# Performance work log

Hardware: AMD Instinct MI355X
Metric: run time of the kernel (lower is better)

## Reference

```python
import jax, jax.numpy as jnp
import numpy as np

PROJ_DIM = 128
TEMP = 0.1
CLAMP_VAL = 50.0
EPS = 1e-6


def _coords(H, W):
    # [H*W, 2] grid of (x, y) coordinates, matching torch meshgrid indexing='ij'
    xs = jnp.arange(W, dtype=jnp.float32)
    ys = jnp.arange(H, dtype=jnp.float32)
    grid_y, grid_x = jnp.meshgrid(ys, xs, indexing='ij')
    return jnp.stack([grid_x.reshape(-1), grid_y.reshape(-1)], axis=-1)


def setup_inputs() -> dict:
    key = jax.random.key(0)
    k1, k2 = jax.random.split(key)
    B, C, H, W = 2, 128, 96, 96
    fL = jax.random.normal(k1, (B, C, H, W), dtype=jnp.float32)
    fR = jax.random.normal(k2, (B, C, H, W), dtype=jnp.float32)
    return {"fL": fL, "fR": fR}


def reference(fL, fR):
    B, C, H, W = fL.shape
    HW = H * W
    scale = jnp.float32(np.sqrt(PROJ_DIM))

    # L2-normalize over channel dim with epsilon clamp
    fLn = fL / jnp.maximum(jnp.linalg.norm(fL, axis=1, keepdims=True), EPS)
    fRn = fR / jnp.maximum(jnp.linalg.norm(fR, axis=1, keepdims=True), EPS)

    q = fLn.reshape(B, C, HW).transpose(0, 2, 1).astype(jnp.float32)  # [B, HW, C]
    k = fRn.reshape(B, C, HW).astype(jnp.float32)                      # [B, C, HW]

    coords = _coords(H, W)  # [HW, 2]

    # Global correlation: [B, HW, HW] (chunking in the original is math-equivalent)
    corr = jnp.einsum('bqc,bck->bqk', q, k) / scale
    corr = jnp.clip(corr / TEMP, -CLAMP_VAL, CLAMP_VAL)
    prob = jax.nn.softmax(corr, axis=-1)

    expected_pos = prob @ coords                 # [B, HW, 2]
    max_prob = jnp.max(prob, axis=-1)            # [B, HW]

    flow_abs = expected_pos.reshape(B, H, W, 2).transpose(0, 3, 1, 2)  # [B, 2, H, W]
    conf = max_prob.reshape(B, 1, H, W)

    src = coords.reshape(H, W, 2).transpose(2, 0, 1)[None]  # [1, 2, H, W]
    flow = (flow_abs - src).astype(fL.dtype)
    conf = conf.astype(fL.dtype)
    return flow, conf
```

## Files before the change

kernel.cpp:

```cpp
#include <hip/hip_runtime.h>
#include <stdint.h>

#define HW 9216
#define CDIM 128
#define WIDTH 96
#define BATCH 2
#define SPLITS 48
#define KSPLIT 192
#define NKG 6
#define QTILE 128
#define NQT (HW / QTILE)
#define NWG (NQT * SPLITS * BATCH)

#define QSCALE 0.44194173824159216f
#define MXSCALE 2.8853900817779268f

typedef _Float16 half8 __attribute__((ext_vector_type(8)));
typedef float f32x16 __attribute__((ext_vector_type(16)));
typedef float float2v __attribute__((ext_vector_type(2)));

__global__ __launch_bounds__(256) void norm_kernel(const float* __restrict__ fL,
                                                   const float* __restrict__ fR,
                                                   _Float16* __restrict__ Qh,
                                                   _Float16* __restrict__ Kh)
{
    __shared__ float ssred[4][64];
    __shared__ _Float16 ot[64 * 130];

    const float* src = (blockIdx.y == 0) ? fL : fR;
    _Float16* dst    = (blockIdx.y == 0) ? Qh : Kh;
    const float outScale = (blockIdx.y == 0) ? QSCALE : 1.0f;

    const int t = threadIdx.x;
    const int pos_l = t & 63, cg = t >> 6;
    const int pos0 = blockIdx.x * 64;
    const int b = pos0 / HW, pos_in = pos0 % HW + pos_l;

    const float* p = src + (size_t)b * CDIM * HW + pos_in;

    float v[32];
    float ss = 0.f;
    #pragma unroll
    for (int j = 0; j < 32; ++j) {
        v[j] = p[(size_t)(cg * 32 + j) * HW];
        ss += v[j] * v[j];
    }
    ssred[cg][pos_l] = ss;
    __syncthreads();
    float tot = ssred[0][pos_l] + ssred[1][pos_l] + ssred[2][pos_l] + ssred[3][pos_l];
    float scale = outScale / fmaxf(sqrtf(tot), 1e-6f);

    #pragma unroll
    for (int j = 0; j < 32; ++j)
        ot[pos_l * 130 + cg * 32 + j] = (_Float16)(v[j] * scale);
    __syncthreads();

    uint4* og = (uint4*)(dst + (size_t)(b * HW + pos0 % HW + 0) * CDIM);
    #pragma unroll
    for (int i = 0; i < 4; ++i) {
        int idx = i * 256 + t;
        int row = idx >> 4, chunk = idx & 15;
        og[idx] = *(const uint4*)&ot[row * 130 + chunk * 8];
    }
}

__global__ __launch_bounds__(256, 3) void attn_kernel(const _Float16* __restrict__ Qh,
                                                      const _Float16* __restrict__ Kh,
                                                      float4* __restrict__ part)
{
    __shared__ __align__(16) _Float16 Ks[KSPLIT * 128];

    const int wg0 = blockIdx.x;
    const int nid = (wg0 & 7) * (NWG / 8) + (wg0 >> 3);
    const int qt = nid % NQT;
    const int sb = nid / NQT;
    const int split = sb % SPLITS;
    const int b = sb / SPLITS;

    const int t = threadIdx.x;
    const int lane = t & 63, wave = t >> 6;
    const int lane31 = lane & 31, hi = lane >> 5;
    const int ln15 = lane & 15, qd = lane >> 4;

    const char* kp0 = (const char*)(Kh + (size_t)b * HW * CDIM) +
                      (size_t)(split * KSPLIT) * (CDIM * 2);

    {
        int voff4[4];
        #pragma unroll
        for (int i = 0; i < 4; ++i) {
            int r = wave * 48 + i * 4 + qd;
            voff4[i] = r * 256 + ((ln15 ^ (r & 15)) << 4) - i * 1024;
        }
        _Float16* db = &Ks[wave * (48 * 128)];
        #pragma unroll
        for (int i = 0; i < 12; ++i)
            __builtin_amdgcn_global_load_lds(
                (const __attribute__((address_space(1))) uint32_t*)(kp0 + voff4[i & 3] + i * 1024),
                (__attribute__((address_space(3))) uint32_t*)(db + i * 512),
                16, 0, 0);
    }

    half8 qf[8];
    {
        const char* qb = (const char*)(Qh +
            ((size_t)(b * HW + qt * QTILE + wave * 32 + lane31)) * CDIM);
        #pragma unroll
        for (int kc = 0; kc < 8; ++kc)
            qf[kc] = *(const half8*)(qb + kc * 32 + hi * 16);
    }

    int rdoff[8];
    #pragma unroll
    for (int kc = 0; kc < 8; ++kc)
        rdoff[kc] = (lane31 << 8) + ((((kc << 1) | hi) ^ ln15) << 4);

    const float ysp = (float)(split * 2);

    float2v E2[8];
    #pragma unroll
    for (int p = 0; p < 8; ++p) E2[p] = (float2v)0.f;
    float mxs = -1.0e30f;
    float2v axb2 = (float2v)0.f, ay2 = (float2v)0.f;

    const char* ksb = (const char*)&Ks[0];
    const float2v C4 = (float2v)(1.0f / 24.0f), C3 = (float2v)(1.0f / 6.0f),
                  C2 = (float2v)0.5f, C1 = (float2v)1.0f;

    __syncthreads();

    #define CHAIN(ACC, KG)                                                       \
        {                                                                        \
            __builtin_amdgcn_s_setprio(1);                                       \
            _Pragma("unroll")                                                    \
            for (int kc = 0; kc < 8; ++kc) {                                     \
                half8 kf = *(const half8*)(ksb + (KG) * 8192 + rdoff[kc]);       \
                ACC = __builtin_amdgcn_mfma_f32_32x32x16_f16(                    \
                    kf, qf[kc], (kc == 0) ? (f32x16)0.f : ACC, 0, 0, 0);         \
            }                                                                    \
            __builtin_amdgcn_s_setprio(0);                                       \
        }

    #define EPI(ACC, KG)                                                         \
        {                                                                        \
            const float xb = (float)(32 * ((KG) % 3));                           \
            const float yk = ysp + (float)((KG) / 3);                            \
            float2v lt2;                                                         \
            _Pragma("unroll")                                                    \
            for (int p = 0; p < 8; ++p) {                                        \
                float2v w;                                                       \
                w.x = ACC[2 * p];                                                \
                w.y = ACC[2 * p + 1];                                            \
                mxs = fmaxf(mxs, fmaxf(w.x, w.y));           \
                float2v h = w * C4 + C3;                       \
                h = h * w + C2;                                                  \
                h = h * w + C1;                                                  \
                h = h * w + C1;                                                  \
                float2v e = h * h;                                               \
                E2[p] += e;                                                      \
                lt2 = (p == 0) ? e : (lt2 + e);                                  \
            }                                                                    \
            axb2 += lt2 * (float2v)xb;                                           \
            ay2  += lt2 * (float2v)yk;                                           \
        }

    f32x16 accA, accB;
    CHAIN(accA, 0)
    CHAIN(accB, 1) __builtin_amdgcn_sched_barrier(0); EPI(accA, 0)
    CHAIN(accA, 2) __builtin_amdgcn_sched_barrier(0); EPI(accB, 1)
    CHAIN(accB, 3) __builtin_amdgcn_sched_barrier(0); EPI(accA, 2)
    CHAIN(accA, 4) __builtin_amdgcn_sched_barrier(0); EPI(accB, 3)
    CHAIN(accB, 5) __builtin_amdgcn_sched_barrier(0); EPI(accA, 4)
    EPI(accB, 5)
    #undef CHAIN
    #undef EPI

    float l = 0.f, axc = 0.f;
    #pragma unroll
    for (int p = 0; p < 8; ++p) {
        const float c0 = (float)(((2 * p) & 3) + 8 * ((2 * p) >> 2));
        l   += E2[p].x + E2[p].y;
        axc += c0 * E2[p].x + (c0 + 1.0f) * E2[p].y;
    }
    float ax = axc + (float)(4 * hi) * l + axb2.x + axb2.y;
    float ay = ay2.x + ay2.y;
    float mx = mxs;

    l  += __shfl_xor(l, 32, 64);
    ax += __shfl_xor(ax, 32, 64);
    ay += __shfl_xor(ay, 32, 64);
    mx  = fmaxf(mx, __shfl_xor(mx, 32, 64));

    if (hi == 0) {
        int row = qt * QTILE + wave * 32 + lane31;
        part[(size_t)split * (BATCH * HW) + b * HW + row] =
            make_float4(l, ax, ay, __builtin_amdgcn_exp2f(mx * MXSCALE));
    }
}

__global__ __launch_bounds__(256) void combine_kernel(const float4* __restrict__ part,
                                                      float* __restrict__ out)
{
    int tid = blockIdx.x * 256 + threadIdx.x;
    int b = tid / HW, pos = tid % HW;
    float l = 0.f, ax = 0.f, ay = 0.f, mx = 0.f;
    #pragma unroll
    for (int s = 0; s < SPLITS; ++s) {
        float4 v = part[(size_t)s * (BATCH * HW) + tid];
        l += v.x; ax += v.y; ay += v.z; mx = fmaxf(mx, v.w);
    }
    float inv = 1.0f / l;
    int x = pos % WIDTH, y = pos / WIDTH;
    out[(size_t)b * 2 * HW + pos]           = ax * inv - (float)x;
    out[(size_t)b * 2 * HW + HW + pos]      = ay * inv - (float)y;
    out[(size_t)BATCH * 2 * HW + (size_t)b * HW + pos] = mx * inv;
}

extern "C" void kernel_launch(void* const* d_in, const int* in_sizes, int n_in,
                              void* d_out, int out_size, void* d_ws, size_t ws_size,
                              hipStream_t stream)
{
    const float* fL = (const float*)d_in[0];
    const float* fR = (const float*)d_in[1];
    float* out = (float*)d_out;

    char* ws = (char*)d_ws;
    const size_t QH_BYTES = (size_t)BATCH * HW * CDIM * sizeof(_Float16);
    _Float16* Qh  = (_Float16*)ws;
    _Float16* Kh  = (_Float16*)(ws + QH_BYTES);
    float4*   part = (float4*)(ws + 2 * QH_BYTES);

    norm_kernel<<<dim3((BATCH * HW) / 64, 2), 256, 0, stream>>>(fL, fR, Qh, Kh);
    attn_kernel<<<dim3(NWG), 256, 0, stream>>>(Qh, Kh, part);
    combine_kernel<<<dim3((BATCH * HW) / 256), 256, 0, stream>>>(part, out);
}
```

Measured before the change: 138.4 us.

## Interleave paired MFMA chains in attention and split combine reduction across waves

The attention kernel now runs two independent MFMA accumulator chains side by side (four accumulators in total) and batches the softmax epilogues into pairs. This exposes more instruction-level parallelism to hide MFMA latency, at the cost of more live registers and possibly lower occupancy. The combine kernel now spreads the 48 split partials over four waves per row group and reduces them through shared memory, launching four times as many blocks so more loads are in flight.

```diff
diff --git a/kernel.cpp b/kernel.cpp
--- a/kernel.cpp
+++ b/kernel.cpp
@@ -129,14 +129,17 @@
 
     __syncthreads();
 
-    #define CHAIN(ACC, KG)                                                       \
+    #define CHAIN2(ACCX, KGX, ACCY, KGY)                                         \
         {                                                                        \
             __builtin_amdgcn_s_setprio(1);                                       \
             _Pragma("unroll")                                                    \
             for (int kc = 0; kc < 8; ++kc) {                                     \
-                half8 kf = *(const half8*)(ksb + (KG) * 8192 + rdoff[kc]);       \
-                ACC = __builtin_amdgcn_mfma_f32_32x32x16_f16(                    \
-                    kf, qf[kc], (kc == 0) ? (f32x16)0.f : ACC, 0, 0, 0);         \
+                half8 kx = *(const half8*)(ksb + (KGX) * 8192 + rdoff[kc]);      \
+                half8 ky = *(const half8*)(ksb + (KGY) * 8192 + rdoff[kc]);      \
+                ACCX = __builtin_amdgcn_mfma_f32_32x32x16_f16(                   \
+                    kx, qf[kc], (kc == 0) ? (f32x16)0.f : ACCX, 0, 0, 0);        \
+                ACCY = __builtin_amdgcn_mfma_f32_32x32x16_f16(                   \
+                    ky, qf[kc], (kc == 0) ? (f32x16)0.f : ACCY, 0, 0, 0);        \
             }                                                                    \
             __builtin_amdgcn_s_setprio(0);                                       \
         }
@@ -164,15 +167,14 @@
             ay2  += lt2 * (float2v)yk;                                           \
         }
 
-    f32x16 accA, accB;
-    CHAIN(accA, 0)
-    CHAIN(accB, 1) __builtin_amdgcn_sched_barrier(0); EPI(accA, 0)
-    CHAIN(accA, 2) __builtin_amdgcn_sched_barrier(0); EPI(accB, 1)
-    CHAIN(accB, 3) __builtin_amdgcn_sched_barrier(0); EPI(accA, 2)
-    CHAIN(accA, 4) __builtin_amdgcn_sched_barrier(0); EPI(accB, 3)
-    CHAIN(accB, 5) __builtin_amdgcn_sched_barrier(0); EPI(accA, 4)
-    EPI(accB, 5)
-    #undef CHAIN
+    f32x16 accA, accB, accC, accD;
+    CHAIN2(accA, 0, accB, 1)
+    CHAIN2(accC, 2, accD, 3)
+    __builtin_amdgcn_sched_barrier(0); EPI(accA, 0) EPI(accB, 1)
+    CHAIN2(accA, 4, accB, 5)
+    __builtin_amdgcn_sched_barrier(0); EPI(accC, 2) EPI(accD, 3)
+    EPI(accA, 4) EPI(accB, 5)
+    #undef CHAIN2
     #undef EPI
 
     float l = 0.f, axc = 0.f;
@@ -201,19 +203,32 @@
 __global__ __launch_bounds__(256) void combine_kernel(const float4* __restrict__ part,
                                                       float* __restrict__ out)
 {
-    int tid = blockIdx.x * 256 + threadIdx.x;
-    int b = tid / HW, pos = tid % HW;
+    __shared__ float4 red[3][64];
+    const int t = threadIdx.x;
+    const int r = t & 63, g = t >> 6;
+    const int tid = blockIdx.x * 64 + r;
+    const int b = tid / HW, pos = tid % HW;
+
     float l = 0.f, ax = 0.f, ay = 0.f, mx = 0.f;
     #pragma unroll
-    for (int s = 0; s < SPLITS; ++s) {
-        float4 v = part[(size_t)s * (BATCH * HW) + tid];
+    for (int s = 0; s < 12; ++s) {
+        float4 v = part[(size_t)(g * 12 + s) * (BATCH * HW) + tid];
         l += v.x; ax += v.y; ay += v.z; mx = fmaxf(mx, v.w);
     }
-    float inv = 1.0f / l;
-    int x = pos % WIDTH, y = pos / WIDTH;
-    out[(size_t)b * 2 * HW + pos]           = ax * inv - (float)x;
-    out[(size_t)b * 2 * HW + HW + pos]      = ay * inv - (float)y;
-    out[(size_t)BATCH * 2 * HW + (size_t)b * HW + pos] = mx * inv;
+    if (g > 0) red[g - 1][r] = make_float4(l, ax, ay, mx);
+    __syncthreads();
+    if (g == 0) {
+        #pragma unroll
+        for (int i = 0; i < 3; ++i) {
+            float4 v = red[i][r];
+            l += v.x; ax += v.y; ay += v.z; mx = fmaxf(mx, v.w);
+        }
+        float inv = 1.0f / l;
+        int x = pos % WIDTH, y = pos / WIDTH;
+        out[(size_t)b * 2 * HW + pos]                      = ax * inv - (float)x;
+        out[(size_t)b * 2 * HW + HW + pos]                 = ay * inv - (float)y;
+        out[(size_t)BATCH * 2 * HW + (size_t)b * HW + pos] = mx * inv;
+    }
 }
 
 extern "C" void kernel_launch(void* const* d_in, const int* in_sizes, int n_in,
@@ -232,5 +247,5 @@
 
     norm_kernel<<<dim3((BATCH * HW) / 64, 2), 256, 0, stream>>>(fL, fR, Qh, Kh);
     attn_kernel<<<dim3(NWG), 256, 0, stream>>>(Qh, Kh, part);
-    combine_kernel<<<dim3((BATCH * HW) / 256), 256, 0, stream>>>(part, out);
-}
+    combine_kernel<<<dim3((BATCH * HW) / 64), 256, 0, stream>>>(part, out);
+}
```

Measured after the change: 141.7 us. +2.5%, slower.
